# Kernel optimization log

Hardware: AMD Instinct MI355X
Metric: run time of the kernel (lower is better)

The kernel has to match this reference:

```python
import jax, jax.numpy as jnp
import numpy as np

B, D3, L, H, O, E, GH = 4096, 288, 32, 512, 96, 8, 128


def _init_linear(key, out_dim, in_dim):
    kw, kb = jax.random.split(key)
    bound = 1.0 / np.sqrt(in_dim)
    W = jax.random.uniform(kw, (out_dim, in_dim), jnp.float32, -bound, bound)
    b = jax.random.uniform(kb, (out_dim,), jnp.float32, -bound, bound)
    return W, b


def setup_inputs() -> dict:
    key = jax.random.key(0)
    ks = jax.random.split(key, 12)
    x = jax.random.normal(ks[0], (B, D3), jnp.float32)
    z = jax.random.normal(ks[1], (B, L), jnp.float32)
    # per-expert weights, stacked on leading expert axis [E, out, in]
    def expert_stack(k, out_dim, in_dim):
        Ws, bs = [], []
        for i in range(E):
            Wi, bi = _init_linear(jax.random.fold_in(k, i), out_dim, in_dim)
            Ws.append(Wi); bs.append(bi)
        return jnp.stack(Ws), jnp.stack(bs)
    W0, b0 = expert_stack(ks[2], H, D3 + L)
    W1, b1 = expert_stack(ks[3], H, H + L)
    W2, b2 = expert_stack(ks[4], H, H + L)
    W3, b3 = expert_stack(ks[5], O, H)
    gW1, gb1 = _init_linear(ks[6], GH, D3 + L)
    gW2, gb2 = _init_linear(ks[7], GH, GH)
    gW3, gb3 = _init_linear(ks[8], E, GH)
    return {"x": x, "z": z, "W0": W0, "b0": b0, "W1": W1, "b1": b1,
            "W2": W2, "b2": b2, "W3": W3, "b3": b3,
            "gW1": gW1, "gb1": gb1, "gW2": gW2, "gb2": gb2,
            "gW3": gW3, "gb3": gb3}


def _gating(x, z, gW1, gb1, gW2, gb2, gW3, gb3):
    h = jnp.concatenate([x, z], axis=1)
    h = jax.nn.elu(h @ gW1.T + gb1)
    h = jax.nn.elu(h @ gW2.T + gb2)
    return jax.nn.softmax(h @ gW3.T + gb3, axis=-1)  # [B, E]


def _blended_linear(g, W, b, h):
    # Original: materializes sum_e g[b,e] * W_e -> [B,out,in], then bmm.
    # Mathematically identical linear form: sum_e g[b,e] * (W_e h_b + b_e).
    return jnp.einsum('be,eoi,bi->bo', g, W, h) + g @ b


def reference(x, z, W0, b0, W1, b1, W2, b2, W3, b3,
              gW1, gb1, gW2, gb2, gW3, gb3):
    g = _gating(x, z, gW1, gb1, gW2, gb2, gW3, gb3)  # [B, E]
    # dropout p=0.0 (eval) -> identity
    h = jax.nn.elu(_blended_linear(g, W0, b0, jnp.concatenate([x, z], axis=1)))
    h = jax.nn.elu(_blended_linear(g, W1, b1, jnp.concatenate([h, z], axis=1)))
    h = jax.nn.elu(_blended_linear(g, W2, b2, jnp.concatenate([h, z], axis=1)))
    out = _blended_linear(g, W3, b3, h)
    return out  # [B, O]
```

## Files before the change

kernel.cpp:

```cpp
#include <hip/hip_runtime.h>
#include <hip/hip_fp16.h>

typedef _Float16 half8 __attribute__((ext_vector_type(8)));
typedef _Float16 half4 __attribute__((ext_vector_type(4)));
typedef float floatx4 __attribute__((ext_vector_type(4)));

__device__ __forceinline__ void async_ld16(const void* g, void* l) {
    __builtin_amdgcn_global_load_lds(
        (const __attribute__((address_space(1))) char*)g,
        (__attribute__((address_space(3))) char*)l, 16, 0, 0);
}

__device__ __forceinline__ float elu_f(float v) {
    return v > 0.f ? v : (__expf(v) - 1.f);
}

__device__ __forceinline__ half4 cvt4(const float* src, int j4) {
    float4 f = ((const float4*)src)[j4];
    half4 h; h.x = (_Float16)f.x; h.y = (_Float16)f.y;
    h.z = (_Float16)f.z; h.w = (_Float16)f.w; return h;
}

__launch_bounds__(256)
__global__ void convert_all(const float* __restrict__ x, const float* __restrict__ z,
                            const float* __restrict__ W0, const float* __restrict__ W1,
                            const float* __restrict__ W2, const float* __restrict__ W3,
                            const float* __restrict__ gW1, const float* __restrict__ gW2,
                            const float* __restrict__ gW3,
                            _Float16* __restrict__ X0,
                            _Float16* __restrict__ h0, _Float16* __restrict__ h1,
                            _Float16* __restrict__ h2,
                            _Float16* __restrict__ Wc0, _Float16* __restrict__ Wc1,
                            _Float16* __restrict__ Wc2, _Float16* __restrict__ Wc3,
                            _Float16* __restrict__ gW1c, _Float16* __restrict__ gW2c,
                            _Float16* __restrict__ gW3c)
{
    const int S0 = 294912;
    const int S1 = 32768;
    const int S2 = 327680;
    const int S3 = 589824;
    const int S4 = 589824;
    const int S5 = 98304;
    const int S6 = 196608;
    const int S7 = 10240;
    const int S8 = 4096;
    const int TOTAL = S0 + S1 + S2 + S3 + S4 + S5 + S6 + S7 + S8 + 256;
    const half4 hz = {};

    for (int i = blockIdx.x * blockDim.x + threadIdx.x; i < TOTAL;
         i += gridDim.x * blockDim.x) {
        int j = i;
        if (j < S0) {
            int r = j / 72, c = j - r * 72;
            *(half4*)(X0 + r * 320 + c * 4) = cvt4(x, j);
            continue;
        }
        j -= S0;
        if (j < S1) {
            int r = j / 8, c = j - r * 8;
            *(half4*)(X0 + r * 320 + 288 + c * 4) = cvt4(z, j);
            continue;
        }
        j -= S1;
        if (j < S2) { *(half4*)(Wc0 + j * 4) = cvt4(W0, j); continue; }
        j -= S2;
        if (j < S3) {
            int r = j / 144, c = j - r * 144;
            *(half4*)(Wc1 + r * 576 + c * 4) = (c < 136) ? cvt4(W1, r * 136 + c) : hz;
            continue;
        }
        j -= S3;
        if (j < S4) {
            int r = j / 144, c = j - r * 144;
            *(half4*)(Wc2 + r * 576 + c * 4) = (c < 136) ? cvt4(W2, r * 136 + c) : hz;
            continue;
        }
        j -= S4;
        if (j < S5) { *(half4*)(Wc3 + j * 4) = cvt4(W3, j); continue; }
        j -= S5;
        if (j < S6) {
            int buf = j >> 16;
            int r2 = j & 65535;
            int row = r2 >> 4, c = r2 & 15;
            _Float16* h = (buf == 0) ? h0 : ((buf == 1) ? h1 : h2);
            *(half4*)(h + row * 576 + 512 + c * 4) = (c < 8) ? cvt4(z, row * 8 + c) : hz;
            continue;
        }
        j -= S6;
        if (j < S7) { *(half4*)(gW1c + j * 4) = cvt4(gW1, j); continue; }
        j -= S7;
        if (j < S8) { *(half4*)(gW2c + j * 4) = cvt4(gW2, j); continue; }
        j -= S8;
        *(half4*)(gW3c + j * 4) = cvt4(gW3, j);
    }
}

__launch_bounds__(256)
__global__ void gating_fast(const _Float16* __restrict__ X0,
                            const _Float16* __restrict__ gW1c,
                            const _Float16* __restrict__ gW2c,
                            const _Float16* __restrict__ gW3c,
                            const float* __restrict__ gb1,
                            const float* __restrict__ gb2,
                            const float* __restrict__ gb3,
                            float* __restrict__ g)
{
    __shared__ _Float16 Tbuf[4 * 16 * 136];

    const int tid = threadIdx.x;
    const int l = tid & 63;
    const int w = tid >> 6;
    const int quad = l >> 4;
    const int mi = l & 15;
    const int kq = quad * 8;
    const int mrow = (blockIdx.x * 4 + w) * 16;

    _Float16* T = Tbuf + w * (16 * 136);
    const _Float16* arow = X0 + (size_t)(mrow + mi) * 320;

    floatx4 acc1[8] = {};
    half8 a_nxt = *(const half8*)(arow + kq);
#pragma unroll
    for (int kc = 0; kc < 10; kc++) {
        const int k0 = kc * 32;
        half8 a = a_nxt;
        if (kc < 9) a_nxt = *(const half8*)(arow + k0 + 32 + kq);
#pragma unroll
        for (int t = 0; t < 8; t++) {
            half8 b = *(const half8*)(gW1c + (size_t)(t * 16 + mi) * 320 + k0 + kq);
            acc1[t] = __builtin_amdgcn_mfma_f32_16x16x32_f16(a, b, acc1[t], 0, 0, 0);
        }
    }
#pragma unroll
    for (int t = 0; t < 8; t++) {
        const int n = t * 16 + mi;
        const float bn = gb1[n];
#pragma unroll
        for (int r = 0; r < 4; r++)
            T[(quad * 4 + r) * 136 + n] = (_Float16)elu_f(acc1[t][r] + bn);
    }

    floatx4 acc2[8] = {};
#pragma unroll
    for (int kc = 0; kc < 4; kc++) {
        const int k0 = kc * 32;
        half8 a = *(const half8*)(T + mi * 136 + k0 + kq);
#pragma unroll
        for (int t = 0; t < 8; t++) {
            half8 b = *(const half8*)(gW2c + (size_t)(t * 16 + mi) * 128 + k0 + kq);
            acc2[t] = __builtin_amdgcn_mfma_f32_16x16x32_f16(a, b, acc2[t], 0, 0, 0);
        }
    }
#pragma unroll
    for (int t = 0; t < 8; t++) {
        const int n = t * 16 + mi;
        const float bn = gb2[n];
#pragma unroll
        for (int r = 0; r < 4; r++)
            T[(quad * 4 + r) * 136 + n] = (_Float16)elu_f(acc2[t][r] + bn);
    }

    floatx4 acc3 = {};
#pragma unroll
    for (int kc = 0; kc < 4; kc++) {
        const int k0 = kc * 32;
        half8 a = *(const half8*)(T + mi * 136 + k0 + kq);
        half8 b = (mi < 8) ? *(const half8*)(gW3c + (size_t)mi * 128 + k0 + kq) : half8{};
        acc3 = __builtin_amdgcn_mfma_f32_16x16x32_f16(a, b, acc3, 0, 0, 0);
    }
    const float gb = gb3[mi & 7];
#pragma unroll
    for (int r = 0; r < 4; r++) {
        float logit = acc3[r] + gb;
        float mx = logit;
        mx = fmaxf(mx, __shfl_xor(mx, 1));
        mx = fmaxf(mx, __shfl_xor(mx, 2));
        mx = fmaxf(mx, __shfl_xor(mx, 4));
        float e = __expf(logit - mx);
        float s = e;
        s += __shfl_xor(s, 1);
        s += __shfl_xor(s, 2);
        s += __shfl_xor(s, 4);
        if (mi < 8)
            g[(size_t)(mrow + quad * 4 + r) * 8 + mi] = e / s;
    }
}

template <bool ELU_ACT, bool SWZ, typename OUT_T>
__launch_bounds__(256, 4)
__global__ void blend64(const _Float16* __restrict__ A, int lda,
                        const _Float16* __restrict__ W, int ldw,
                        int Hdim, int K,
                        const float* __restrict__ g,
                        const float* __restrict__ bias,
                        OUT_T* __restrict__ out, int ldo)
{
    __shared__ __align__(16) char smem_raw[32768];
    _Float16* sA = (_Float16*)smem_raw;
    _Float16* sB = (_Float16*)(smem_raw + 16384);
    float* sredf = (float*)smem_raw;
    __shared__ float sg[128][9];
    __shared__ float sbias[8][16];

    const int tid = threadIdx.x;
    const int l = tid & 63;
    const int w = tid >> 6;
    const int wm = w >> 1, wn = w & 1;

    int by, bx;
    if (SWZ) {
        const int id = blockIdx.x;
        const int r = id & 7, q = id >> 3;
        by = (r >> 1) * 8 + (q & 7);
        bx = (r & 1) * 16 + (q >> 3);
    } else {
        const int id = blockIdx.x;
        by = id / 6;
        bx = id - by * 6;
    }
    const int o0 = bx * 16;
    const int m0 = by * 128;

    for (int t = tid; t < 128 * 8; t += 256)
        sg[t >> 3][t & 7] = g[(size_t)(m0 + (t >> 3)) * 8 + (t & 7)];
    for (int t = tid; t < 128; t += 256)
        sbias[t >> 4][t & 15] = bias[(t >> 4) * Hdim + o0 + (t & 15)];

    const int lr = l >> 3;
    const int lc = l & 7;
    const int swz = lc ^ lr;

    const _Float16* gAp = A + (size_t)(m0 + w * 64 + lr) * lda + swz * 8;
    _Float16* lAp = sA + w * 4096;
    const int wb = w - 2;
    const int eb = wb * 4;
    const _Float16* gBe = W + ((size_t)eb * Hdim + o0 + lr) * ldw + swz * 8;
    const _Float16* gBo = gBe + (size_t)8 * ldw;
    _Float16* lBp = sB + wb * 4096;

    const int mi = l & 15, quad = l >> 4;
    const int cswz = mi & 7;
    const int offh0 = ((quad ^ cswz) * 8);
    const int offh1 = (((quad + 4) ^ cswz) * 8);
    const _Float16* rAb = sA + (wm * 64 + mi) * 64;
    const _Float16* rBb = sB + (wn * 64 + mi) * 64;

    floatx4 acc[4][4] = {};

    for (int k0 = 0; k0 < K; k0 += 64) {
        __syncthreads();
        if (w < 2) {
            const _Float16* gp = gAp + k0;
            _Float16* lp = lAp;
#pragma unroll
            for (int c = 0; c < 8; c++) {
                async_ld16(gp, lp);
                gp += (size_t)8 * lda;
                lp += 512;
            }
        } else {
            const _Float16* ge = gBe + k0;
            const _Float16* go = gBo + k0;
            _Float16* lp = lBp;
#pragma unroll
            for (int c2 = 0; c2 < 4; c2++) {
                async_ld16(ge, lp); lp += 512;
                async_ld16(go, lp); lp += 512;
                ge += (size_t)Hdim * ldw;
                go += (size_t)Hdim * ldw;
            }
        }
        __syncthreads();
#pragma unroll
        for (int h = 0; h < 2; h++) {
            const int off = h ? offh1 : offh0;
            half8 af[4], bf[4];
#pragma unroll
            for (int i = 0; i < 4; i++) af[i] = *(const half8*)(rAb + i * 1024 + off);
#pragma unroll
            for (int j = 0; j < 4; j++) bf[j] = *(const half8*)(rBb + j * 1024 + off);
#pragma unroll
            for (int i = 0; i < 4; i++)
#pragma unroll
                for (int j = 0; j < 4; j++)
                    acc[i][j] = __builtin_amdgcn_mfma_f32_16x16x32_f16(af[i], bf[j], acc[i][j], 0, 0, 0);
        }
    }

    float p[4][4];
#pragma unroll
    for (int i = 0; i < 4; i++)
#pragma unroll
        for (int r = 0; r < 4; r++) {
            int mloc = wm * 64 + i * 16 + quad * 4 + r;
            float s = 0.f;
#pragma unroll
            for (int j = 0; j < 4; j++) {
                int e = wn * 4 + j;
                s += sg[mloc][e] * (acc[i][j][r] + sbias[e][mi]);
            }
            p[i][r] = s;
        }

    __syncthreads();
    if (wn == 0) {
#pragma unroll
        for (int i = 0; i < 4; i++)
#pragma unroll
            for (int r = 0; r < 4; r++)
                sredf[(wm * 64 + i * 16 + quad * 4 + r) * 17 + mi] = p[i][r];
    }
    __syncthreads();
    if (wn == 1) {
#pragma unroll
        for (int i = 0; i < 4; i++)
#pragma unroll
            for (int r = 0; r < 4; r++) {
                int mrel = i * 16 + quad * 4 + r;
                float v = p[i][r] + sredf[(wm * 64 + mrel) * 17 + mi];
                if (ELU_ACT) v = elu_f(v);
                out[(size_t)(m0 + wm * 64 + mrel) * ldo + o0 + mi] = (OUT_T)v;
            }
    }
}

extern "C" void kernel_launch(void* const* d_in, const int* in_sizes, int n_in,
                              void* d_out, int out_size, void* d_ws, size_t ws_size,
                              hipStream_t stream)
{
    (void)in_sizes; (void)n_in; (void)out_size; (void)ws_size;
    const float* x   = (const float*)d_in[0];
    const float* z   = (const float*)d_in[1];
    const float* W0  = (const float*)d_in[2];
    const float* b0  = (const float*)d_in[3];
    const float* W1  = (const float*)d_in[4];
    const float* b1  = (const float*)d_in[5];
    const float* W2  = (const float*)d_in[6];
    const float* b2  = (const float*)d_in[7];
    const float* W3  = (const float*)d_in[8];
    const float* b3  = (const float*)d_in[9];
    const float* gW1 = (const float*)d_in[10];
    const float* gb1 = (const float*)d_in[11];
    const float* gW2 = (const float*)d_in[12];
    const float* gb2 = (const float*)d_in[13];
    const float* gW3 = (const float*)d_in[14];
    const float* gb3 = (const float*)d_in[15];

    char* p = (char*)d_ws;
    auto alloc = [&](size_t n) { char* r = p; p += (n + 255) & ~(size_t)255; return r; };
    _Float16* X0   = (_Float16*)alloc((size_t)4096 * 320 * 2);
    _Float16* h0   = (_Float16*)alloc((size_t)4096 * 576 * 2);
    _Float16* h1   = (_Float16*)alloc((size_t)4096 * 576 * 2);
    _Float16* h2   = (_Float16*)alloc((size_t)4096 * 576 * 2);
    _Float16* Wc0  = (_Float16*)alloc((size_t)8 * 512 * 320 * 2);
    _Float16* Wc1  = (_Float16*)alloc((size_t)8 * 512 * 576 * 2);
    _Float16* Wc2  = (_Float16*)alloc((size_t)8 * 512 * 576 * 2);
    _Float16* Wc3  = (_Float16*)alloc((size_t)8 * 96 * 512 * 2);
    _Float16* gW1c = (_Float16*)alloc((size_t)128 * 320 * 2);
    _Float16* gW2c = (_Float16*)alloc((size_t)128 * 128 * 2);
    _Float16* gW3c = (_Float16*)alloc((size_t)8 * 128 * 2);
    float*    g    = (float*)alloc((size_t)4096 * 8 * 4);

    convert_all<<<1024, 256, 0, stream>>>(x, z, W0, W1, W2, W3, gW1, gW2, gW3,
                                          X0, h0, h1, h2, Wc0, Wc1, Wc2, Wc3,
                                          gW1c, gW2c, gW3c);

    gating_fast<<<64, 256, 0, stream>>>(X0, gW1c, gW2c, gW3c, gb1, gb2, gb3, g);

    blend64<true, true, _Float16><<<1024, 256, 0, stream>>>(X0, 320, Wc0, 320, 512, 320, g, b0, h0, 576);
    blend64<true, true, _Float16><<<1024, 256, 0, stream>>>(h0, 576, Wc1, 576, 512, 576, g, b1, h1, 576);
    blend64<true, true, _Float16><<<1024, 256, 0, stream>>>(h1, 576, Wc2, 576, 512, 576, g, b2, h2, 576);
    blend64<false, false, float><<<192, 256, 0, stream>>>(h2, 576, Wc3, 512, 96, 512, g, b3, (float*)d_out, 96);
}
```

Before: 191.9 us.

## Enlarge blend kernel to 256-row tiles with 512 threads and shared loading

Replaces the 128-row, 256-thread blended-linear kernel with a 256-row, 512-thread version in which every wave loads part of both the activation and weight tiles, instead of splitting waves into A-loaders and B-loaders. Each weight tile staged in LDS is now reused across twice as many rows, which should cut global and L2 weight traffic and halve the number of blocks. The block-swizzle mapping and grid sizes are adjusted to match. Gating weights are now held in LDS as fp16, which gives a small precision loss. The larger block uses more LDS and has fewer blocks in flight, which may lower occupancy.

Result: no change. 189.1 us (-1.5%).

```diff
diff --git a/kernel.cpp b/kernel.cpp
--- a/kernel.cpp
+++ b/kernel.cpp
@@ -187,19 +187,19 @@
 }
 
 template <bool ELU_ACT, bool SWZ, typename OUT_T>
-__launch_bounds__(256, 4)
-__global__ void blend64(const _Float16* __restrict__ A, int lda,
-                        const _Float16* __restrict__ W, int ldw,
-                        int Hdim, int K,
-                        const float* __restrict__ g,
-                        const float* __restrict__ bias,
-                        OUT_T* __restrict__ out, int ldo)
+__launch_bounds__(512, 4)
+__global__ void blend256(const _Float16* __restrict__ A, int lda,
+                         const _Float16* __restrict__ W, int ldw,
+                         int Hdim, int K,
+                         const float* __restrict__ g,
+                         const float* __restrict__ bias,
+                         OUT_T* __restrict__ out, int ldo)
 {
-    __shared__ __align__(16) char smem_raw[32768];
+    __shared__ __align__(16) char smem_raw[49152];
     _Float16* sA = (_Float16*)smem_raw;
-    _Float16* sB = (_Float16*)(smem_raw + 16384);
+    _Float16* sB = (_Float16*)(smem_raw + 32768);
     float* sredf = (float*)smem_raw;
-    __shared__ float sg[128][9];
+    __shared__ _Float16 sg[256][8];
     __shared__ float sbias[8][16];
 
     const int tid = threadIdx.x;
@@ -211,69 +211,53 @@
     if (SWZ) {
         const int id = blockIdx.x;
         const int r = id & 7, q = id >> 3;
-        by = (r >> 1) * 8 + (q & 7);
-        bx = (r & 1) * 16 + (q >> 3);
+        by = (r >> 1) * 4 + (q & 3);
+        bx = (r & 1) * 16 + (q >> 2);
     } else {
         const int id = blockIdx.x;
         by = id / 6;
         bx = id - by * 6;
     }
     const int o0 = bx * 16;
-    const int m0 = by * 128;
-
-    for (int t = tid; t < 128 * 8; t += 256)
-        sg[t >> 3][t & 7] = g[(size_t)(m0 + (t >> 3)) * 8 + (t & 7)];
-    for (int t = tid; t < 128; t += 256)
-        sbias[t >> 4][t & 15] = bias[(t >> 4) * Hdim + o0 + (t & 15)];
+    const int m0 = by * 256;
+
+    for (int t = tid; t < 256 * 8; t += 512)
+        sg[t >> 3][t & 7] = (_Float16)g[(size_t)(m0 + (t >> 3)) * 8 + (t & 7)];
+    if (tid < 128)
+        sbias[tid >> 4][tid & 15] = bias[(tid >> 4) * Hdim + o0 + (tid & 15)];
 
     const int lr = l >> 3;
     const int lc = l & 7;
     const int swz = lc ^ lr;
 
-    const _Float16* gAp = A + (size_t)(m0 + w * 64 + lr) * lda + swz * 8;
-    _Float16* lAp = sA + w * 4096;
-    const int wb = w - 2;
-    const int eb = wb * 4;
-    const _Float16* gBe = W + ((size_t)eb * Hdim + o0 + lr) * ldw + swz * 8;
-    const _Float16* gBo = gBe + (size_t)8 * ldw;
-    _Float16* lBp = sB + wb * 4096;
+    const _Float16* gAp = A + (size_t)(m0 + w * 32 + lr) * lda + swz * 8;
+    _Float16* const lAp = sA + w * 2048;
+    const _Float16* gBp = W + ((size_t)w * Hdim + o0 + lr) * ldw + swz * 8;
+    _Float16* const lBp = sB + w * 1024;
 
     const int mi = l & 15, quad = l >> 4;
     const int cswz = mi & 7;
-    const int offh0 = ((quad ^ cswz) * 8);
-    const int offh1 = (((quad + 4) ^ cswz) * 8);
-    const _Float16* rAb = sA + (wm * 64 + mi) * 64;
-    const _Float16* rBb = sB + (wn * 64 + mi) * 64;
+    const _Float16* const rAb = sA + (wm * 64 + mi) * 64;
+    const _Float16* const rBb = sB + (wn * 64 + mi) * 64;
 
     floatx4 acc[4][4] = {};
 
     for (int k0 = 0; k0 < K; k0 += 64) {
         __syncthreads();
-        if (w < 2) {
-            const _Float16* gp = gAp + k0;
-            _Float16* lp = lAp;
-#pragma unroll
-            for (int c = 0; c < 8; c++) {
-                async_ld16(gp, lp);
-                gp += (size_t)8 * lda;
-                lp += 512;
-            }
-        } else {
-            const _Float16* ge = gBe + k0;
-            const _Float16* go = gBo + k0;
-            _Float16* lp = lBp;
-#pragma unroll
-            for (int c2 = 0; c2 < 4; c2++) {
-                async_ld16(ge, lp); lp += 512;
-                async_ld16(go, lp); lp += 512;
-                ge += (size_t)Hdim * ldw;
-                go += (size_t)Hdim * ldw;
-            }
+        {
+            const _Float16* ga = gAp + k0;
+#pragma unroll
+            for (int c = 0; c < 4; c++)
+                async_ld16(ga + (size_t)c * 8 * lda, lAp + c * 512);
+            const _Float16* gb = gBp + k0;
+#pragma unroll
+            for (int c = 0; c < 2; c++)
+                async_ld16(gb + (size_t)c * 8 * ldw, lBp + c * 512);
         }
         __syncthreads();
 #pragma unroll
         for (int h = 0; h < 2; h++) {
-            const int off = h ? offh1 : offh0;
+            const int off = ((h * 4 + quad) ^ cswz) * 8;
             half8 af[4], bf[4];
 #pragma unroll
             for (int i = 0; i < 4; i++) af[i] = *(const half8*)(rAb + i * 1024 + off);
@@ -292,12 +276,12 @@
     for (int i = 0; i < 4; i++)
 #pragma unroll
         for (int r = 0; r < 4; r++) {
-            int mloc = wm * 64 + i * 16 + quad * 4 + r;
+            const int mloc = wm * 64 + i * 16 + quad * 4 + r;
             float s = 0.f;
 #pragma unroll
             for (int j = 0; j < 4; j++) {
-                int e = wn * 4 + j;
-                s += sg[mloc][e] * (acc[i][j][r] + sbias[e][mi]);
+                const int e = wn * 4 + j;
+                s += (float)sg[mloc][e] * (acc[i][j][r] + sbias[e][mi]);
             }
             p[i][r] = s;
         }
@@ -316,10 +300,10 @@
         for (int i = 0; i < 4; i++)
 #pragma unroll
             for (int r = 0; r < 4; r++) {
-                int mrel = i * 16 + quad * 4 + r;
-                float v = p[i][r] + sredf[(wm * 64 + mrel) * 17 + mi];
+                const int mrel = wm * 64 + i * 16 + quad * 4 + r;
+                float v = p[i][r] + sredf[mrel * 17 + mi];
                 if (ELU_ACT) v = elu_f(v);
-                out[(size_t)(m0 + wm * 64 + mrel) * ldo + o0 + mi] = (OUT_T)v;
+                out[(size_t)(m0 + mrel) * ldo + o0 + mi] = (OUT_T)v;
             }
     }
 }
@@ -367,8 +351,8 @@
 
     gating_fast<<<64, 256, 0, stream>>>(X0, gW1c, gW2c, gW3c, gb1, gb2, gb3, g);
 
-    blend64<true, true, _Float16><<<1024, 256, 0, stream>>>(X0, 320, Wc0, 320, 512, 320, g, b0, h0, 576);
-    blend64<true, true, _Float16><<<1024, 256, 0, stream>>>(h0, 576, Wc1, 576, 512, 576, g, b1, h1, 576);
-    blend64<true, true, _Float16><<<1024, 256, 0, stream>>>(h1, 576, Wc2, 576, 512, 576, g, b2, h2, 576);
-    blend64<false, false, float><<<192, 256, 0, stream>>>(h2, 576, Wc3, 512, 96, 512, g, b3, (float*)d_out, 96);
-}
+    blend256<true, true, _Float16><<<512, 512, 0, stream>>>(X0, 320, Wc0, 320, 512, 320, g, b0, h0, 576);
+    blend256<true, true, _Float16><<<512, 512, 0, stream>>>(h0, 576, Wc1, 576, 512, 576, g, b1, h1, 576);
+    blend256<true, true, _Float16><<<512, 512, 0, stream>>>(h1, 576, Wc2, 576, 512, 576, g, b2, h2, 576);
+    blend256<false, false, float><<<96, 512, 0, stream>>>(h2, 576, Wc3, 512, 96, 512, g, b3, (float*)d_out, 96);
+}
```
